# Kernel optimization log

Measured on AMD Instinct MI355X. Metric: run time of the kernel, lower is better.

The kernel has to match this reference:

```python
import jax, jax.numpy as jnp
import numpy as np

N, E = 50000, 800000
IN_DIM, HID, HEADS, OUT_DIM, EDGE_DIM = 128, 32, 4, 64, 32


def _glorot(key, shape, dtype=jnp.float32):
    fan_in, fan_out = shape[0], shape[1]
    lim = np.sqrt(6.0 / (fan_in + fan_out))
    return jax.random.uniform(key, shape, dtype, -lim, lim)


def setup_inputs() -> dict:
    key = jax.random.key(0)
    ks = jax.random.split(key, 16)
    H1 = HEADS * HID  # 128 = concat width of layer 1
    inp = {
        "x": jax.random.normal(ks[0], (N, IN_DIM), jnp.float32),
        "edge_index": jax.random.randint(ks[1], (2, E), 0, N, jnp.int64),
        "edge_feats": jax.random.normal(ks[2], (E, EDGE_DIM), jnp.float32),
        # layer 1: TransformerConv(128 -> 32, heads=4, concat=True, edge_dim=32)
        "Wq1": _glorot(ks[3], (IN_DIM, H1)), "bq1": jnp.zeros((H1,), jnp.float32),
        "Wk1": _glorot(ks[4], (IN_DIM, H1)), "bk1": jnp.zeros((H1,), jnp.float32),
        "Wv1": _glorot(ks[5], (IN_DIM, H1)), "bv1": jnp.zeros((H1,), jnp.float32),
        "We1": _glorot(ks[6], (EDGE_DIM, H1)),
        "Ws1": _glorot(ks[7], (IN_DIM, H1)), "bs1": jnp.zeros((H1,), jnp.float32),
        # layer 2: TransformerConv(128 -> 64, heads=1, concat=False, edge_dim=32)
        "Wq2": _glorot(ks[8], (H1, OUT_DIM)), "bq2": jnp.zeros((OUT_DIM,), jnp.float32),
        "Wk2": _glorot(ks[9], (H1, OUT_DIM)), "bk2": jnp.zeros((OUT_DIM,), jnp.float32),
        "Wv2": _glorot(ks[10], (H1, OUT_DIM)), "bv2": jnp.zeros((OUT_DIM,), jnp.float32),
        "We2": _glorot(ks[11], (EDGE_DIM, OUT_DIM)),
        "Ws2": _glorot(ks[12], (H1, OUT_DIM)), "bs2": jnp.zeros((OUT_DIM,), jnp.float32),
    }
    return inp


def _tconv(x, src, dst, e, Wq, bq, Wk, bk, Wv, bv, We, Ws, bs, heads, concat):
    """PyG TransformerConv: gather q_i/k_j/v_j, add edge embedding to k and v,
    segment-softmax over incoming edges of each target node, scatter-aggregate."""
    n = x.shape[0]
    d = Wq.shape[1] // heads
    q = (x @ Wq + bq).reshape(n, heads, d)
    k = (x @ Wk + bk).reshape(n, heads, d)
    v = (x @ Wv + bv).reshape(n, heads, d)
    ee = (e @ We).reshape(-1, heads, d)      # [E, H, D]
    kj = k[src] + ee                          # [E, H, D]
    vj = v[src] + ee                          # [E, H, D]
    a = jnp.einsum('ehd,ehd->eh', q[dst], kj) / jnp.sqrt(jnp.asarray(d, x.dtype))
    amax = jax.ops.segment_max(a, dst, num_segments=n)      # [N, H]
    ex = jnp.exp(a - amax[dst])
    den = jax.ops.segment_sum(ex, dst, num_segments=n)
    alpha = ex / den[dst]                                   # [E, H]
    out = jax.ops.segment_sum(alpha[..., None] * vj, dst, num_segments=n)
    out = out.reshape(n, heads * d) if concat else out.mean(axis=1)
    return out + x @ Ws + bs  # root/skip connection (lin_skip)


def reference(x, edge_index, edge_feats,
              Wq1, bq1, Wk1, bk1, Wv1, bv1, We1, Ws1, bs1,
              Wq2, bq2, Wk2, bk2, Wv2, bv2, We2, Ws2, bs2):
    src, dst = edge_index[0], edge_index[1]  # flow='source_to_target'
    h = _tconv(x, src, dst, edge_feats, Wq1, bq1, Wk1, bk1, Wv1, bv1,
               We1, Ws1, bs1, heads=HEADS, concat=True)
    h = jax.nn.relu(h)  # activation; dropout p=0.0 is identity
    h = _tconv(h, src, dst, edge_feats, Wq2, bq2, Wk2, bk2, Wv2, bv2,
               We2, Ws2, bs2, heads=1, concat=False)
    return h
```

## Files before the change

kernel.cpp:

```cpp
#include <hip/hip_runtime.h>
#include <hip/hip_bf16.h>


typedef unsigned int  u32;
typedef unsigned short u16;
typedef __attribute__((ext_vector_type(8))) __bf16 bf16x8;
typedef __attribute__((ext_vector_type(4))) float  f32x4;

#define S1L (0.17677669529663687f * 1.4426950408889634f)
#define S2L (0.125f * 1.4426950408889634f)

__device__ __forceinline__ u16 f2bf(float f) {
    u32 u = __float_as_uint(f);
    u32 r = (u + 0x7fffu + ((u >> 16) & 1u)) >> 16;
    return (u16)r;
}
__device__ __forceinline__ float bflo(u32 u) { return __uint_as_float(u << 16); }
__device__ __forceinline__ float bfhi(u32 u) { return __uint_as_float(u & 0xffff0000u); }

template<int CTRL>
__device__ __forceinline__ float dpp_add(float x) {
    int y = __builtin_amdgcn_mov_dpp(__float_as_int(x), CTRL, 0xF, 0xF, true);
    return x + __int_as_float(y);
}

__global__ void k_hist(const int* __restrict__ dst, int* __restrict__ deg, int nE) {
    int e = blockIdx.x * 256 + threadIdx.x;
    if (e < nE) atomicAdd(&deg[dst[e]], 1);
}

__global__ __launch_bounds__(1024) void k_scan_part(const int* __restrict__ deg,
                                                    int* __restrict__ rp,
                                                    int* __restrict__ csum, int nN)
{
    __shared__ int buf[1024];
    const int tid = threadIdx.x, idx = blockIdx.x * 1024 + tid;
    int v = (idx < nN) ? deg[idx] : 0;
    buf[tid] = v;
    __syncthreads();
    for (int off = 1; off < 1024; off <<= 1) {
        int t = (tid >= off) ? buf[tid - off] : 0;
        __syncthreads();
        buf[tid] += t;
        __syncthreads();
    }
    if (idx < nN) rp[idx] = buf[tid] - v;
    if (tid == 1023) csum[blockIdx.x] = buf[1023];
}

__global__ __launch_bounds__(1024) void k_scan_tot(int* __restrict__ csum, int nb,
                                                   int* __restrict__ rowptr, int nN, int nE)
{
    __shared__ int buf[1024];
    const int tid = threadIdx.x;
    int v = (tid < nb) ? csum[tid] : 0;
    buf[tid] = v;
    __syncthreads();
    for (int off = 1; off < 1024; off <<= 1) {
        int t = (tid >= off) ? buf[tid - off] : 0;
        __syncthreads();
        buf[tid] += t;
        __syncthreads();
    }
    if (tid < nb) csum[tid] = buf[tid] - v;
    if (tid == 0) rowptr[nN] = nE;
}

__global__ void k_scan_apply(int* __restrict__ rp, const int* __restrict__ csum,
                             int* __restrict__ fill, int nN)
{
    int i = blockIdx.x * 256 + threadIdx.x;
    if (i < nN) { int r = rp[i] + csum[i >> 10]; rp[i] = r; fill[i] = r; }
}

__global__ void k_scatter_idx(const int* __restrict__ src, const int* __restrict__ dst,
                              int* __restrict__ fill, int2* __restrict__ se, int nE)
{
    int e = blockIdx.x * 256 + threadIdx.x;
    if (e < nE) {
        int p = atomicAdd(&fill[dst[e]], 1);
        se[p] = make_int2(src[e], e);
    }
}

__global__ void k_ef_gather(const int2* __restrict__ se, const float4* __restrict__ ef4,
                            uint2* __restrict__ efc2, int nE)
{
    int t = blockIdx.x * 256 + threadIdx.x;
    int p = t >> 3, sub = t & 7;
    if (p >= nE) return;
    int e = se[p].y;
    float4 f = ef4[(size_t)e * 8 + sub];
    efc2[(size_t)p * 8 + sub] =
        make_uint2((u32)f2bf(f.x) | ((u32)f2bf(f.y) << 16),
                   (u32)f2bf(f.z) | ((u32)f2bf(f.w) << 16));
}

__global__ void k_prep(
    const float* __restrict__ Wq1, const float* __restrict__ Wk1,
    const float* __restrict__ Wv1, const float* __restrict__ Ws1,
    const float* __restrict__ Wq2, const float* __restrict__ Wk2,
    const float* __restrict__ Wv2, const float* __restrict__ Ws2,
    const float* __restrict__ We1, const float* __restrict__ We2,
    const float* __restrict__ bq1, const float* __restrict__ bq2,
    u16* __restrict__ WB1, u16* __restrict__ WB2,
    float* __restrict__ bqe1, float* __restrict__ bqe2,
    const float4* __restrict__ x4, uint2* __restrict__ xb4, int nN)
{
    long t = (long)blockIdx.x * 256 + threadIdx.x;
    if (t < 65536) {
        int j = (int)t >> 7, k = (int)t & 127;
        int m = j >> 7, col = j & 127;
        const float* W = (m == 0) ? Wq1 : (m == 1) ? Wk1 : (m == 2) ? Wv1 : Ws1;
        WB1[t] = f2bf(W[k * 128 + col]);
        return;
    }
    t -= 65536;
    if (t < 49152) {
        int j = (int)t >> 7, k = (int)t & 127;
        if (j < 256) {
            int m = j >> 6, col = j & 63;
            const float* W = (m == 0) ? Wq2 : (m == 1) ? Wk2 : (m == 2) ? Wv2 : Ws2;
            WB2[t] = f2bf(W[k * 64 + col]);
        } else if (j >= 288) {
            WB2[t] = 0;
        }
        return;
    }
    t -= 49152;
    if (t < 16384) {
        int j = (int)t >> 7, m = (int)t & 127;
        int h = j >> 5, c = j & 31;
        float acc = 0.f;
        #pragma unroll
        for (int d = 0; d < 32; ++d)
            acc += Wq1[m * 128 + h * 32 + d] * We1[c * 128 + h * 32 + d];
        WB1[512 * 128 + j * 128 + m] = f2bf(acc * S1L);
        if (m == 0) {
            float b = 0.f;
            #pragma unroll
            for (int d = 0; d < 32; ++d)
                b += bq1[h * 32 + d] * We1[c * 128 + h * 32 + d];
            bqe1[j] = b * S1L;
        }
        return;
    }
    t -= 16384;
    if (t < 4096) {
        int c = (int)t >> 7, m = (int)t & 127;
        float acc = 0.f;
        #pragma unroll
        for (int d = 0; d < 64; ++d)
            acc += Wq2[m * 64 + d] * We2[c * 64 + d];
        WB2[256 * 128 + c * 128 + m] = f2bf(acc * S2L);
        if (m == 0) {
            float b = 0.f;
            #pragma unroll
            for (int d = 0; d < 64; ++d) b += bq2[d] * We2[c * 64 + d];
            bqe2[c] = b * S2L;
        }
        return;
    }
    t -= 4096;
    if (t < (long)nN * 32) {
        float4 f = x4[t];
        xb4[t] = make_uint2((u32)f2bf(f.x) | ((u32)f2bf(f.y) << 16),
                            (u32)f2bf(f.z) | ((u32)f2bf(f.w) << 16));
    }
}

__global__ __launch_bounds__(256) void k_lin_gemm1(
    const u16* __restrict__ xb, const u16* __restrict__ WB,
    const float* __restrict__ bq, const float* __restrict__ bk,
    const float* __restrict__ bv, const float* __restrict__ bs,
    const float* __restrict__ bqe,
    u32* __restrict__ qqe1, u32* __restrict__ kv1, float* __restrict__ sk1, int nN)
{
    __shared__ __align__(16) u16 lds[2 * 128 * 128];
    const int tid = threadIdx.x;
    const int ct = blockIdx.y;
    const int rowbase = blockIdx.x * 128;

    {
        const int lr = tid >> 4, kc = tid & 15;
        #pragma unroll
        for (int it = 0; it < 8; ++it) {
            int row = it * 16 + lr;
            int grow = rowbase + row; if (grow >= nN) grow = nN - 1;
            uint4 va = *(const uint4*)(xb + (size_t)grow * 128 + kc * 8);
            *(uint4*)((char*)lds + row * 256 + ((kc * 16) ^ ((row & 7) << 4))) = va;
        }
        #pragma unroll
        for (int it = 0; it < 8; ++it) {
            int row = it * 16 + lr;
            uint4 vb = *(const uint4*)(WB + ((size_t)ct * 128 + row) * 128 + kc * 8);
            *(uint4*)((char*)lds + 32768 + row * 256 + ((kc * 16) ^ ((row & 7) << 4))) = vb;
        }
    }
    __syncthreads();

    const int wave = tid >> 6, lane = tid & 63;
    const int wr = wave >> 1, wc = wave & 1;
    const int colL = lane & 15, kgrp = lane >> 4;

    f32x4 acc[4][4];
    #pragma unroll
    for (int m = 0; m < 4; ++m)
        #pragma unroll
        for (int n = 0; n < 4; ++n) acc[m][n] = {0.f, 0.f, 0.f, 0.f};

    #pragma unroll
    for (int ks = 0; ks < 4; ++ks) {
        const int kb = ks * 64 + kgrp * 16;
        bf16x8 af[4], bfr[4];
        #pragma unroll
        for (int m = 0; m < 4; ++m) {
            int row = wr * 64 + m * 16 + colL;
            af[m] = *(const bf16x8*)((const char*)lds + row * 256 + (kb ^ ((row & 7) << 4)));
        }
        #pragma unroll
        for (int n = 0; n < 4; ++n) {
            int row = wc * 64 + n * 16 + colL;
            bfr[n] = *(const bf16x8*)((const char*)lds + 32768 + row * 256 + (kb ^ ((row & 7) << 4)));
        }
        #pragma unroll
        for (int m = 0; m < 4; ++m)
            #pragma unroll
            for (int n = 0; n < 4; ++n)
                acc[m][n] = __builtin_amdgcn_mfma_f32_16x16x32_bf16(af[m], bfr[n], acc[m][n], 0, 0, 0);
    }

    const float* bias = (ct == 0) ? bq : (ct == 1) ? bk : (ct == 2) ? bv : (ct == 3) ? bs : bqe;
    const float scale = (ct == 0) ? S1L : 1.f;
    const bool  is32 = (ct == 3);
    const int   hi = (ct == 2 || ct == 4) ? 1 : 0;
    u32* dstw = (ct == 3) ? (u32*)sk1 : ((ct == 1 || ct == 2) ? kv1 : qqe1);

    #pragma unroll
    for (int n = 0; n < 4; ++n) {
        const int c = wc * 64 + n * 16 + colL;
        const float bval = bias[c];
        #pragma unroll
        for (int m = 0; m < 4; ++m) {
            #pragma unroll
            for (int i = 0; i < 4; ++i) {
                const int r = rowbase + wr * 64 + m * 16 + kgrp * 4 + i;
                if (r < nN) {
                    float v = (acc[m][n][i] + bval) * scale;
                    if (is32) ((float*)dstw)[(size_t)r * 128 + c] = v;
                    else ((u16*)dstw)[(((size_t)r * 128 + c) << 1) + hi] = f2bf(v);
                }
            }
        }
    }
}

__global__ __launch_bounds__(256) void k_lin_gemm2(
    const u16* __restrict__ hb, const u16* __restrict__ WB,
    const float* __restrict__ bq, const float* __restrict__ bk,
    const float* __restrict__ bv, const float* __restrict__ bs,
    const float* __restrict__ bqe,
    float* __restrict__ q2, u32* __restrict__ kv2, float* __restrict__ sk2,
    float* __restrict__ qe2, int nN)
{
    __shared__ __align__(16) u16 lds[2 * 128 * 128];
    const int tid = threadIdx.x;
    const int ct = blockIdx.y;
    const int rowbase = blockIdx.x * 128;

    {
        const int lr = tid >> 4, kc = tid & 15;
        #pragma unroll
        for (int it = 0; it < 8; ++it) {
            int row = it * 16 + lr;
            int grow = rowbase + row; if (grow >= nN) grow = nN - 1;
            uint4 va = *(const uint4*)(hb + (size_t)grow * 128 + kc * 8);
            *(uint4*)((char*)lds + row * 256 + ((kc * 16) ^ ((row & 7) << 4))) = va;
        }
        #pragma unroll
        for (int it = 0; it < 8; ++it) {
            int row = it * 16 + lr;
            uint4 vb = *(const uint4*)(WB + ((size_t)ct * 128 + row) * 128 + kc * 8);
            *(uint4*)((char*)lds + 32768 + row * 256 + ((kc * 16) ^ ((row & 7) << 4))) = vb;
        }
    }
    __syncthreads();

    const int wave = tid >> 6, lane = tid & 63;
    const int wr = wave >> 1, wc = wave & 1;
    const int colL = lane & 15, kgrp = lane >> 4;

    f32x4 acc[4][4];
    #pragma unroll
    for (int m = 0; m < 4; ++m)
        #pragma unroll
        for (int n = 0; n < 4; ++n) acc[m][n] = {0.f, 0.f, 0.f, 0.f};

    #pragma unroll
    for (int ks = 0; ks < 4; ++ks) {
        const int kb = ks * 64 + kgrp * 16;
        bf16x8 af[4], bfr[4];
        #pragma unroll
        for (int m = 0; m < 4; ++m) {
            int row = wr * 64 + m * 16 + colL;
            af[m] = *(const bf16x8*)((const char*)lds + row * 256 + (kb ^ ((row & 7) << 4)));
        }
        #pragma unroll
        for (int n = 0; n < 4; ++n) {
            int row = wc * 64 + n * 16 + colL;
            bfr[n] = *(const bf16x8*)((const char*)lds + 32768 + row * 256 + (kb ^ ((row & 7) << 4)));
        }
        #pragma unroll
        for (int m = 0; m < 4; ++m)
            #pragma unroll
            for (int n = 0; n < 4; ++n)
                acc[m][n] = __builtin_amdgcn_mfma_f32_16x16x32_bf16(af[m], bfr[n], acc[m][n], 0, 0, 0);
    }

    const int mode = ct * 2 + wc;
    if (mode == 5) return;

    #pragma unroll
    for (int n = 0; n < 4; ++n) {
        const int cl = n * 16 + colL;
        float bval;
        if (mode == 0) bval = bq[cl];
        else if (mode == 1) bval = bk[cl];
        else if (mode == 2) bval = bv[cl];
        else if (mode == 3) bval = bs[cl];
        else bval = (cl < 32) ? bqe[cl] : 0.f;
        #pragma unroll
        for (int m = 0; m < 4; ++m) {
            #pragma unroll
            for (int i = 0; i < 4; ++i) {
                const int r = rowbase + wr * 64 + m * 16 + kgrp * 4 + i;
                if (r < nN) {
                    const float v = acc[m][n][i] + bval;
                    if (mode == 0)      q2[(size_t)r * 64 + cl] = v * S2L;
                    else if (mode == 1) ((u16*)kv2)[(((size_t)r * 64 + cl) << 1)] = f2bf(v);
                    else if (mode == 2) ((u16*)kv2)[(((size_t)r * 64 + cl) << 1) + 1] = f2bf(v);
                    else if (mode == 3) sk2[(size_t)r * 64 + cl] = v;
                    else if (cl < 32)   qe2[(size_t)r * 32 + cl] = v;
                }
            }
        }
    }
}

__global__ __launch_bounds__(256) void k_agg1(
    const int* __restrict__ rowptr, const int2* __restrict__ se,
    const u16* __restrict__ efc, const u32* __restrict__ qqe1,
    const u32* __restrict__ kv1,
    float* __restrict__ sv1, float* __restrict__ sef1, float* __restrict__ den1, int nN)
{
    const int wave = threadIdx.x >> 6, lane = threadIdx.x & 63;
    const int d = blockIdx.x * 4 + wave;
    if (d >= nN) return;
    const int es = lane >> 5;
    const int h  = (lane >> 3) & 3;
    const int c8 = lane & 7;
    const int jb = h * 32 + c8 * 4;

    const uint4 qq = *(const uint4*)(qqe1 + (size_t)d * 128 + jb);
    const float4 qr  = {bflo(qq.x), bflo(qq.y), bflo(qq.z), bflo(qq.w)};
    const float4 qer = {bfhi(qq.x), bfhi(qq.y), bfhi(qq.z), bfhi(qq.w)};

    const int beg = rowptr[d], end = rowptr[d + 1];
    float den = 0.f;
    float4 sv = {0.f, 0.f, 0.f, 0.f}, sef = sv;

    for (int cbeg = beg; cbeg < end; cbeg += 64) {
        const int cnt = min(64, end - cbeg);
        const int sreg = se[cbeg + (lane < cnt ? lane : cnt - 1)].x;
        #pragma unroll 2
        for (int t = 0; t < cnt; t += 2) {
            const int idx = t + es;
            const bool valid = idx < cnt;
            const int s = __shfl(sreg, idx);
            const int iec = cbeg + (valid ? idx : 0);
            const uint4 kp = *(const uint4*)(kv1 + ((u32)s << 7) + jb);
            const uint2 ee = *(const uint2*)(efc + ((size_t)iec << 5) + c8 * 4);
            const float f0 = bflo(ee.x), f1 = bfhi(ee.x);
            const float f2 = bflo(ee.y), f3 = bfhi(ee.y);
            float p = qr.x * bflo(kp.x) + qr.y * bflo(kp.y)
                    + qr.z * bflo(kp.z) + qr.w * bflo(kp.w)
                    + qer.x * f0 + qer.y * f1 + qer.z * f2 + qer.w * f3;
            p = dpp_add<0xB1>(p);
            p = dpp_add<0x4E>(p);
            p = dpp_add<0x141>(p);
            const float ex = valid ? exp2f(p) : 0.f;
            den += ex;
            sv.x += ex * bfhi(kp.x); sv.y += ex * bfhi(kp.y);
            sv.z += ex * bfhi(kp.z); sv.w += ex * bfhi(kp.w);
            sef.x += ex * f0; sef.y += ex * f1; sef.z += ex * f2; sef.w += ex * f3;
        }
    }
    den  += __shfl_xor(den, 32);
    sv.x += __shfl_xor(sv.x, 32); sv.y += __shfl_xor(sv.y, 32);
    sv.z += __shfl_xor(sv.z, 32); sv.w += __shfl_xor(sv.w, 32);
    sef.x += __shfl_xor(sef.x, 32); sef.y += __shfl_xor(sef.y, 32);
    sef.z += __shfl_xor(sef.z, 32); sef.w += __shfl_xor(sef.w, 32);
    if (es == 0) {
        *(float4*)(sv1  + (size_t)d * 128 + jb) = sv;
        *(float4*)(sef1 + (size_t)d * 128 + jb) = sef;
        if (c8 == 0) den1[(size_t)d * 4 + h] = den;
    }
}

__global__ __launch_bounds__(256) void k_finalize1(
    const float* __restrict__ sv1, const float* __restrict__ sef1,
    const float* __restrict__ den1, const float* __restrict__ sk1,
    const float* __restrict__ We, u16* __restrict__ h1b, int nN)
{
    const int tid = threadIdx.x;
    const int g = tid >> 7, j = tid & 127, h = j >> 5;
    float wreg[32];
    #pragma unroll
    for (int cc = 0; cc < 32; ++cc) wreg[cc] = We[cc * 128 + j];
    for (int n = blockIdx.x * 2 + g; n < nN; n += gridDim.x * 2) {
        float dd = den1[(size_t)n * 4 + h];
        float acc = sv1[(size_t)n * 128 + j];
        const float* sefp = &sef1[(size_t)n * 128 + h * 32];
        #pragma unroll
        for (int cc = 0; cc < 32; ++cc) acc = fmaf(sefp[cc], wreg[cc], acc);
        float o = (dd > 0.f ? acc / dd : 0.f) + sk1[(size_t)n * 128 + j];
        h1b[(size_t)n * 128 + j] = f2bf(o > 0.f ? o : 0.f);
    }
}

__global__ __launch_bounds__(256) void k_agg2(
    const int* __restrict__ rowptr, const int2* __restrict__ se,
    const u16* __restrict__ efc, const float* __restrict__ q2,
    const float* __restrict__ qe2, const u32* __restrict__ kv2,
    float* __restrict__ sv2, float* __restrict__ sef2, float* __restrict__ den2, int nN)
{
    const int wave = threadIdx.x >> 6, lane = threadIdx.x & 63;
    const int d = blockIdx.x * 4 + wave;
    if (d >= nN) return;
    const int es  = lane >> 4;
    const int c16 = lane & 15;
    const int jb  = c16 * 4;
    const int ce  = (c16 & 7) * 4;

    const float4 qr = *(const float4*)(q2 + (size_t)d * 64 + jb);
    float4 qer = {0.f, 0.f, 0.f, 0.f};
    if (c16 < 8) qer = *(const float4*)(qe2 + (size_t)d * 32 + jb);

    const int beg = rowptr[d], end = rowptr[d + 1];
    float den = 0.f;
    float4 sv = {0.f, 0.f, 0.f, 0.f}, sef = sv;

    for (int cbeg = beg; cbeg < end; cbeg += 64) {
        const int cnt = min(64, end - cbeg);
        const int sreg = se[cbeg + (lane < cnt ? lane : cnt - 1)].x;
        #pragma unroll 2
        for (int t = 0; t < cnt; t += 4) {
            const int idx = t + es;
            const bool valid = idx < cnt;
            const int s = __shfl(sreg, idx);
            const int iec = cbeg + (valid ? idx : 0);
            const uint4 kp = *(const uint4*)(kv2 + ((u32)s << 6) + jb);
            const uint2 ee = *(const uint2*)(efc + ((size_t)iec << 5) + ce);
            const float f0 = bflo(ee.x), f1 = bfhi(ee.x);
            const float f2 = bflo(ee.y), f3 = bfhi(ee.y);
            float p = qr.x * bflo(kp.x) + qr.y * bflo(kp.y)
                    + qr.z * bflo(kp.z) + qr.w * bflo(kp.w)
                    + qer.x * f0 + qer.y * f1 + qer.z * f2 + qer.w * f3;
            p = dpp_add<0xB1>(p);
            p = dpp_add<0x4E>(p);
            p = dpp_add<0x141>(p);
            p = dpp_add<0x140>(p);
            const float ex = valid ? exp2f(p) : 0.f;
            den += ex;
            sv.x += ex * bfhi(kp.x); sv.y += ex * bfhi(kp.y);
            sv.z += ex * bfhi(kp.z); sv.w += ex * bfhi(kp.w);
            sef.x += ex * f0; sef.y += ex * f1; sef.z += ex * f2; sef.w += ex * f3;
        }
    }
    #pragma unroll
    for (int m = 16; m <= 32; m <<= 1) {
        den  += __shfl_xor(den, m);
        sv.x += __shfl_xor(sv.x, m); sv.y += __shfl_xor(sv.y, m);
        sv.z += __shfl_xor(sv.z, m); sv.w += __shfl_xor(sv.w, m);
        sef.x += __shfl_xor(sef.x, m); sef.y += __shfl_xor(sef.y, m);
        sef.z += __shfl_xor(sef.z, m); sef.w += __shfl_xor(sef.w, m);
    }
    if (es == 0) {
        *(float4*)(sv2 + (size_t)d * 64 + jb) = sv;
        if (c16 < 8) *(float4*)(sef2 + (size_t)d * 32 + jb) = sef;
        if (c16 == 0) den2[d] = den;
    }
}

__global__ __launch_bounds__(256) void k_finalize2(
    const float* __restrict__ sv2, const float* __restrict__ sef2,
    const float* __restrict__ den2, const float* __restrict__ sk2,
    const float* __restrict__ We, float* __restrict__ out, int nN)
{
    const int tid = threadIdx.x;
    const int g = tid >> 6, c = tid & 63;
    float wreg[32];
    #pragma unroll
    for (int k = 0; k < 32; ++k) wreg[k] = We[k * 64 + c];
    for (int n = blockIdx.x * 4 + g; n < nN; n += gridDim.x * 4) {
        float dd = den2[n];
        float acc = sv2[(size_t)n * 64 + c];
        const float* sefp = &sef2[(size_t)n * 32];
        #pragma unroll
        for (int k = 0; k < 32; ++k) acc = fmaf(sefp[k], wreg[k], acc);
        out[(size_t)n * 64 + c] = (dd > 0.f ? acc / dd : 0.f) + sk2[(size_t)n * 64 + c];
    }
}

extern "C" void kernel_launch(void* const* d_in, const int* in_sizes, int n_in,
                              void* d_out, int out_size, void* d_ws, size_t ws_size,
                              hipStream_t stream)
{
    const float* x   = (const float*)d_in[0];
    const int*   ei  = (const int*)d_in[1];
    const float* ef  = (const float*)d_in[2];
    const float* Wq1 = (const float*)d_in[3];  const float* bq1 = (const float*)d_in[4];
    const float* Wk1 = (const float*)d_in[5];  const float* bk1 = (const float*)d_in[6];
    const float* Wv1 = (const float*)d_in[7];  const float* bv1 = (const float*)d_in[8];
    const float* We1 = (const float*)d_in[9];
    const float* Ws1 = (const float*)d_in[10]; const float* bs1 = (const float*)d_in[11];
    const float* Wq2 = (const float*)d_in[12]; const float* bq2 = (const float*)d_in[13];
    const float* Wk2 = (const float*)d_in[14]; const float* bk2 = (const float*)d_in[15];
    const float* Wv2 = (const float*)d_in[16]; const float* bv2 = (const float*)d_in[17];
    const float* We2 = (const float*)d_in[18];
    const float* Ws2 = (const float*)d_in[19]; const float* bs2 = (const float*)d_in[20];

    const int nN = in_sizes[0] / 128;
    const int nE = in_sizes[1] / 2;
    const int* srcv = ei;
    const int* dstv = ei + nE;

    float* ws = (float*)d_ws;
    size_t off = 0;
    auto alloc = [&](size_t n) { float* p = ws + off; off += n; return p; };
    u32*   qqe1  = (u32*)alloc((size_t)nN * 128);
    float* sk1   = alloc((size_t)nN * 128);
    u32*   kv1   = (u32*)alloc((size_t)nN * 128);
    float* sv1   = alloc((size_t)nN * 128);
    float* sef1  = alloc((size_t)nN * 128);
    u16*   h1b   = (u16*)alloc((size_t)nN * 64);
    u16*   xb    = (u16*)alloc((size_t)nN * 64);
    float* den1  = alloc((size_t)nN * 4);
    u16*   efc   = (u16*)alloc((size_t)nE * 16);
    u16*   WB1   = (u16*)alloc(640 * 128 / 2);
    u16*   WB2   = (u16*)alloc(384 * 128 / 2);
    float* bqe1  = alloc(128);
    float* bqe2  = alloc(32);
    int* deg     = (int*)alloc(nN);
    int* rowptr  = (int*)alloc(nN + 1);
    int* fill    = (int*)alloc(nN);
    int* csum    = (int*)alloc(1024);
    int2* se     = (int2*)alloc((size_t)nE * 2);
    float* l2 = (float*)qqe1;
    size_t o2 = 0;
    auto alloc2 = [&](size_t n) { float* p = l2 + o2; o2 += n; return p; };
    float* q2   = alloc2((size_t)nN * 64);
    u32*   kv2  = (u32*)alloc2((size_t)nN * 64);
    float* sk2  = alloc2((size_t)nN * 64);
    float* qe2  = alloc2((size_t)nN * 32);
    float* sv2  = alloc2((size_t)nN * 64);
    float* sef2 = alloc2((size_t)nN * 32);
    float* den2 = alloc2(nN);
    (void)ws_size; (void)n_in; (void)out_size;

    const int nChunk = (nN + 1023) / 1024;
    const int rowTiles = (nN + 127) / 128;

    hipMemsetAsync(deg, 0, (size_t)nN * sizeof(int), stream);
    k_hist<<<(nE + 255) / 256, 256, 0, stream>>>(dstv, deg, nE);
    k_scan_part<<<nChunk, 1024, 0, stream>>>(deg, rowptr, csum, nN);
    k_scan_tot<<<1, 1024, 0, stream>>>(csum, nChunk, rowptr, nN, nE);
    k_scan_apply<<<(nN + 255) / 256, 256, 0, stream>>>(rowptr, csum, fill, nN);
    k_scatter_idx<<<(nE + 255) / 256, 256, 0, stream>>>(srcv, dstv, fill, se, nE);
    k_ef_gather<<<(nE * 8 + 255) / 256, 256, 0, stream>>>(
        se, (const float4*)ef, (uint2*)efc, nE);

    long prepTotal = 65536L + 49152 + 16384 + 4096 + (long)nN * 32;
    k_prep<<<(int)((prepTotal + 255) / 256), 256, 0, stream>>>(
        Wq1, Wk1, Wv1, Ws1, Wq2, Wk2, Wv2, Ws2, We1, We2, bq1, bq2,
        WB1, WB2, bqe1, bqe2, (const float4*)x, (uint2*)xb, nN);

    k_lin_gemm1<<<dim3(rowTiles, 5), 256, 0, stream>>>(
        xb, WB1, bq1, bk1, bv1, bs1, bqe1, qqe1, kv1, sk1, nN);
    k_agg1<<<(nN + 3) / 4, 256, 0, stream>>>(
        rowptr, se, efc, qqe1, kv1, sv1, sef1, den1, nN);
    k_finalize1<<<1024, 256, 0, stream>>>(sv1, sef1, den1, sk1, We1, h1b, nN);

    k_lin_gemm2<<<dim3(rowTiles, 3), 256, 0, stream>>>(
        h1b, WB2, bq2, bk2, bv2, bs2, bqe2, q2, kv2, sk2, qe2, nN);
    k_agg2<<<(nN + 3) / 4, 256, 0, stream>>>(
        rowptr, se, efc, q2, qe2, kv2, sv2, sef2, den2, nN);
    k_finalize2<<<1024, 256, 0, stream>>>(sv2, sef2, den2, sk2, We2, (float*)d_out, nN);
}
```

Baseline: 405.6 us.

## Fuse finalize into aggregation kernels and merge scatter with prep

Merges the aggregation and finalize stages of both layers into persistent grid-stride kernels. Each wave writes its per-node softmax numerators and denominators to LDS, and the We projection, normalization, skip add and activation are applied in place. This removes the global round trip of sv/sef/den buffers and two launches. The edge-index scatter is also folded into the weight/x prep kernel to save another launch. The cost is two block-wide syncs per iteration, so waves with high-degree nodes stall the whole block, and extra registers are needed to hold We.

New measurement: 402.2 us. No clear change (-0.8%).

```diff
diff --git a/kernel.cpp b/kernel.cpp
--- a/kernel.cpp
+++ b/kernel.cpp
@@ -73,30 +73,9 @@
     if (i < nN) { int r = rp[i] + csum[i >> 10]; rp[i] = r; fill[i] = r; }
 }
 
-__global__ void k_scatter_idx(const int* __restrict__ src, const int* __restrict__ dst,
-                              int* __restrict__ fill, int2* __restrict__ se, int nE)
-{
-    int e = blockIdx.x * 256 + threadIdx.x;
-    if (e < nE) {
-        int p = atomicAdd(&fill[dst[e]], 1);
-        se[p] = make_int2(src[e], e);
-    }
-}
-
-__global__ void k_ef_gather(const int2* __restrict__ se, const float4* __restrict__ ef4,
-                            uint2* __restrict__ efc2, int nE)
-{
-    int t = blockIdx.x * 256 + threadIdx.x;
-    int p = t >> 3, sub = t & 7;
-    if (p >= nE) return;
-    int e = se[p].y;
-    float4 f = ef4[(size_t)e * 8 + sub];
-    efc2[(size_t)p * 8 + sub] =
-        make_uint2((u32)f2bf(f.x) | ((u32)f2bf(f.y) << 16),
-                   (u32)f2bf(f.z) | ((u32)f2bf(f.w) << 16));
-}
-
-__global__ void k_prep(
+__global__ void k_scatter_prep(
+    const int* __restrict__ src, const int* __restrict__ dst,
+    int* __restrict__ fill, int2* __restrict__ se, int nE,
     const float* __restrict__ Wq1, const float* __restrict__ Wk1,
     const float* __restrict__ Wv1, const float* __restrict__ Ws1,
     const float* __restrict__ Wq2, const float* __restrict__ Wk2,
@@ -107,7 +86,14 @@
     float* __restrict__ bqe1, float* __restrict__ bqe2,
     const float4* __restrict__ x4, uint2* __restrict__ xb4, int nN)
 {
-    long t = (long)blockIdx.x * 256 + threadIdx.x;
+    long g = (long)blockIdx.x * 256 + threadIdx.x;
+    if (g < nE) {
+        int e = (int)g;
+        int p = atomicAdd(&fill[dst[e]], 1);
+        se[p] = make_int2(src[e], e);
+        return;
+    }
+    long t = g - nE;
     if (t < 65536) {
         int j = (int)t >> 7, k = (int)t & 127;
         int m = j >> 7, col = j & 127;
@@ -167,6 +153,19 @@
         xb4[t] = make_uint2((u32)f2bf(f.x) | ((u32)f2bf(f.y) << 16),
                             (u32)f2bf(f.z) | ((u32)f2bf(f.w) << 16));
     }
+}
+
+__global__ void k_ef_gather(const int2* __restrict__ se, const float4* __restrict__ ef4,
+                            uint2* __restrict__ efc2, int nE)
+{
+    int t = blockIdx.x * 256 + threadIdx.x;
+    int p = t >> 3, sub = t & 7;
+    if (p >= nE) return;
+    int e = se[p].y;
+    float4 f = ef4[(size_t)e * 8 + sub];
+    efc2[(size_t)p * 8 + sub] =
+        make_uint2((u32)f2bf(f.x) | ((u32)f2bf(f.y) << 16),
+                   (u32)f2bf(f.z) | ((u32)f2bf(f.w) << 16));
 }
 
 __global__ __launch_bounds__(256) void k_lin_gemm1(
@@ -347,168 +346,178 @@
     }
 }
 
-__global__ __launch_bounds__(256) void k_agg1(
+__global__ __launch_bounds__(256) void k_agg1f(
     const int* __restrict__ rowptr, const int2* __restrict__ se,
     const u16* __restrict__ efc, const u32* __restrict__ qqe1,
-    const u32* __restrict__ kv1,
-    float* __restrict__ sv1, float* __restrict__ sef1, float* __restrict__ den1, int nN)
-{
+    const u32* __restrict__ kv1, const float* __restrict__ sk1,
+    const float* __restrict__ We, u16* __restrict__ h1b, int nN, int stride4)
+{
+    __shared__ float lsv[4][128];
+    __shared__ float lsef[4][128];
+    __shared__ float lden[4][4];
     const int wave = threadIdx.x >> 6, lane = threadIdx.x & 63;
-    const int d = blockIdx.x * 4 + wave;
-    if (d >= nN) return;
     const int es = lane >> 5;
     const int h  = (lane >> 3) & 3;
     const int c8 = lane & 7;
     const int jb = h * 32 + c8 * 4;
-
-    const uint4 qq = *(const uint4*)(qqe1 + (size_t)d * 128 + jb);
-    const float4 qr  = {bflo(qq.x), bflo(qq.y), bflo(qq.z), bflo(qq.w)};
-    const float4 qer = {bfhi(qq.x), bfhi(qq.y), bfhi(qq.z), bfhi(qq.w)};
-
-    const int beg = rowptr[d], end = rowptr[d + 1];
-    float den = 0.f;
-    float4 sv = {0.f, 0.f, 0.f, 0.f}, sef = sv;
-
-    for (int cbeg = beg; cbeg < end; cbeg += 64) {
-        const int cnt = min(64, end - cbeg);
-        const int sreg = se[cbeg + (lane < cnt ? lane : cnt - 1)].x;
-        #pragma unroll 2
-        for (int t = 0; t < cnt; t += 2) {
-            const int idx = t + es;
-            const bool valid = idx < cnt;
-            const int s = __shfl(sreg, idx);
-            const int iec = cbeg + (valid ? idx : 0);
-            const uint4 kp = *(const uint4*)(kv1 + ((u32)s << 7) + jb);
-            const uint2 ee = *(const uint2*)(efc + ((size_t)iec << 5) + c8 * 4);
-            const float f0 = bflo(ee.x), f1 = bfhi(ee.x);
-            const float f2 = bflo(ee.y), f3 = bfhi(ee.y);
-            float p = qr.x * bflo(kp.x) + qr.y * bflo(kp.y)
-                    + qr.z * bflo(kp.z) + qr.w * bflo(kp.w)
-                    + qer.x * f0 + qer.y * f1 + qer.z * f2 + qer.w * f3;
-            p = dpp_add<0xB1>(p);
-            p = dpp_add<0x4E>(p);
-            p = dpp_add<0x141>(p);
-            const float ex = valid ? exp2f(p) : 0.f;
-            den += ex;
-            sv.x += ex * bfhi(kp.x); sv.y += ex * bfhi(kp.y);
-            sv.z += ex * bfhi(kp.z); sv.w += ex * bfhi(kp.w);
-            sef.x += ex * f0; sef.y += ex * f1; sef.z += ex * f2; sef.w += ex * f3;
-        }
-    }
-    den  += __shfl_xor(den, 32);
-    sv.x += __shfl_xor(sv.x, 32); sv.y += __shfl_xor(sv.y, 32);
-    sv.z += __shfl_xor(sv.z, 32); sv.w += __shfl_xor(sv.w, 32);
-    sef.x += __shfl_xor(sef.x, 32); sef.y += __shfl_xor(sef.y, 32);
-    sef.z += __shfl_xor(sef.z, 32); sef.w += __shfl_xor(sef.w, 32);
-    if (es == 0) {
-        *(float4*)(sv1  + (size_t)d * 128 + jb) = sv;
-        *(float4*)(sef1 + (size_t)d * 128 + jb) = sef;
-        if (c8 == 0) den1[(size_t)d * 4 + h] = den;
-    }
-}
-
-__global__ __launch_bounds__(256) void k_finalize1(
-    const float* __restrict__ sv1, const float* __restrict__ sef1,
-    const float* __restrict__ den1, const float* __restrict__ sk1,
-    const float* __restrict__ We, u16* __restrict__ h1b, int nN)
-{
-    const int tid = threadIdx.x;
-    const int g = tid >> 7, j = tid & 127, h = j >> 5;
-    float wreg[32];
-    #pragma unroll
-    for (int cc = 0; cc < 32; ++cc) wreg[cc] = We[cc * 128 + j];
-    for (int n = blockIdx.x * 2 + g; n < nN; n += gridDim.x * 2) {
-        float dd = den1[(size_t)n * 4 + h];
-        float acc = sv1[(size_t)n * 128 + j];
-        const float* sefp = &sef1[(size_t)n * 128 + h * 32];
-        #pragma unroll
-        for (int cc = 0; cc < 32; ++cc) acc = fmaf(sefp[cc], wreg[cc], acc);
-        float o = (dd > 0.f ? acc / dd : 0.f) + sk1[(size_t)n * 128 + j];
-        h1b[(size_t)n * 128 + j] = f2bf(o > 0.f ? o : 0.f);
-    }
-}
-
-__global__ __launch_bounds__(256) void k_agg2(
+    const int jA = lane, jB = lane + 64;
+    const int hA = jA >> 5, hB = jB >> 5;
+    float wA[32], wB[32];
+    #pragma unroll
+    for (int c = 0; c < 32; ++c) {
+        wA[c] = We[c * 128 + jA];
+        wB[c] = We[c * 128 + jB];
+    }
+
+    for (int dbase = blockIdx.x * 4; dbase < nN; dbase += stride4) {
+        const int d = dbase + wave;
+        const bool act = d < nN;
+        float den = 0.f;
+        float4 sv = {0.f, 0.f, 0.f, 0.f}, sef = sv;
+        if (act) {
+            const uint4 qq = *(const uint4*)(qqe1 + (size_t)d * 128 + jb);
+            const float4 qr  = {bflo(qq.x), bflo(qq.y), bflo(qq.z), bflo(qq.w)};
+            const float4 qer = {bfhi(qq.x), bfhi(qq.y), bfhi(qq.z), bfhi(qq.w)};
+            const int beg = rowptr[d], end = rowptr[d + 1];
+            for (int cbeg = beg; cbeg < end; cbeg += 64) {
+                const int cnt = min(64, end - cbeg);
+                const int sreg = se[cbeg + (lane < cnt ? lane : cnt - 1)].x;
+                #pragma unroll 2
+                for (int t = 0; t < cnt; t += 2) {
+                    const int idx = t + es;
+                    const bool valid = idx < cnt;
+                    const int s = __shfl(sreg, idx);
+                    const int iec = cbeg + (valid ? idx : 0);
+                    const uint4 kp = *(const uint4*)(kv1 + ((u32)s << 7) + jb);
+                    const uint2 ee = *(const uint2*)(efc + ((size_t)iec << 5) + c8 * 4);
+                    const float f0 = bflo(ee.x), f1 = bfhi(ee.x);
+                    const float f2 = bflo(ee.y), f3 = bfhi(ee.y);
+                    float p = qr.x * bflo(kp.x) + qr.y * bflo(kp.y)
+                            + qr.z * bflo(kp.z) + qr.w * bflo(kp.w)
+                            + qer.x * f0 + qer.y * f1 + qer.z * f2 + qer.w * f3;
+                    p = dpp_add<0xB1>(p);
+                    p = dpp_add<0x4E>(p);
+                    p = dpp_add<0x141>(p);
+                    const float ex = valid ? exp2f(p) : 0.f;
+                    den += ex;
+                    sv.x += ex * bfhi(kp.x); sv.y += ex * bfhi(kp.y);
+                    sv.z += ex * bfhi(kp.z); sv.w += ex * bfhi(kp.w);
+                    sef.x += ex * f0; sef.y += ex * f1; sef.z += ex * f2; sef.w += ex * f3;
+                }
+            }
+            den  += __shfl_xor(den, 32);
+            sv.x += __shfl_xor(sv.x, 32); sv.y += __shfl_xor(sv.y, 32);
+            sv.z += __shfl_xor(sv.z, 32); sv.w += __shfl_xor(sv.w, 32);
+            sef.x += __shfl_xor(sef.x, 32); sef.y += __shfl_xor(sef.y, 32);
+            sef.z += __shfl_xor(sef.z, 32); sef.w += __shfl_xor(sef.w, 32);
+            if (es == 0) {
+                *(float4*)&lsv[wave][jb]  = sv;
+                *(float4*)&lsef[wave][jb] = sef;
+                if (c8 == 0) lden[wave][h] = den;
+            }
+        }
+        __syncthreads();
+        if (act) {
+            const float ddA = lden[wave][hA], ddB = lden[wave][hB];
+            const float invA = ddA > 0.f ? 1.0f / ddA : 0.f;
+            const float invB = ddB > 0.f ? 1.0f / ddB : 0.f;
+            float aA = lsv[wave][jA], aB = lsv[wave][jB];
+            const float* spA = &lsef[wave][hA * 32];
+            const float* spB = &lsef[wave][hB * 32];
+            #pragma unroll
+            for (int c = 0; c < 32; ++c) {
+                aA = fmaf(spA[c], wA[c], aA);
+                aB = fmaf(spB[c], wB[c], aB);
+            }
+            float oA = aA * invA + sk1[(size_t)d * 128 + jA];
+            float oB = aB * invB + sk1[(size_t)d * 128 + jB];
+            h1b[(size_t)d * 128 + jA] = f2bf(oA > 0.f ? oA : 0.f);
+            h1b[(size_t)d * 128 + jB] = f2bf(oB > 0.f ? oB : 0.f);
+        }
+        __syncthreads();
+    }
+}
+
+__global__ __launch_bounds__(256) void k_agg2f(
     const int* __restrict__ rowptr, const int2* __restrict__ se,
     const u16* __restrict__ efc, const float* __restrict__ q2,
     const float* __restrict__ qe2, const u32* __restrict__ kv2,
-    float* __restrict__ sv2, float* __restrict__ sef2, float* __restrict__ den2, int nN)
-{
+    const float* __restrict__ sk2, const float* __restrict__ We,
+    float* __restrict__ out, int nN, int stride4)
+{
+    __shared__ float lsv[4][64];
+    __shared__ float lsef[4][32];
+    __shared__ float lden[4];
     const int wave = threadIdx.x >> 6, lane = threadIdx.x & 63;
-    const int d = blockIdx.x * 4 + wave;
-    if (d >= nN) return;
     const int es  = lane >> 4;
     const int c16 = lane & 15;
     const int jb  = c16 * 4;
     const int ce  = (c16 & 7) * 4;
-
-    const float4 qr = *(const float4*)(q2 + (size_t)d * 64 + jb);
-    float4 qer = {0.f, 0.f, 0.f, 0.f};
-    if (c16 < 8) qer = *(const float4*)(qe2 + (size_t)d * 32 + jb);
-
-    const int beg = rowptr[d], end = rowptr[d + 1];
-    float den = 0.f;
-    float4 sv = {0.f, 0.f, 0.f, 0.f}, sef = sv;
-
-    for (int cbeg = beg; cbeg < end; cbeg += 64) {
-        const int cnt = min(64, end - cbeg);
-        const int sreg = se[cbeg + (lane < cnt ? lane : cnt - 1)].x;
-        #pragma unroll 2
-        for (int t = 0; t < cnt; t += 4) {
-            const int idx = t + es;
-            const bool valid = idx < cnt;
-            const int s = __shfl(sreg, idx);
-            const int iec = cbeg + (valid ? idx : 0);
-            const uint4 kp = *(const uint4*)(kv2 + ((u32)s << 6) + jb);
-            const uint2 ee = *(const uint2*)(efc + ((size_t)iec << 5) + ce);
-            const float f0 = bflo(ee.x), f1 = bfhi(ee.x);
-            const float f2 = bflo(ee.y), f3 = bfhi(ee.y);
-            float p = qr.x * bflo(kp.x) + qr.y * bflo(kp.y)
-                    + qr.z * bflo(kp.z) + qr.w * bflo(kp.w)
-                    + qer.x * f0 + qer.y * f1 + qer.z * f2 + qer.w * f3;
-            p = dpp_add<0xB1>(p);
-            p = dpp_add<0x4E>(p);
-            p = dpp_add<0x141>(p);
-            p = dpp_add<0x140>(p);
-            const float ex = valid ? exp2f(p) : 0.f;
-            den += ex;
-            sv.x += ex * bfhi(kp.x); sv.y += ex * bfhi(kp.y);
-            sv.z += ex * bfhi(kp.z); sv.w += ex * bfhi(kp.w);
-            sef.x += ex * f0; sef.y += ex * f1; sef.z += ex * f2; sef.w += ex * f3;
-        }
-    }
-    #pragma unroll
-    for (int m = 16; m <= 32; m <<= 1) {
-        den  += __shfl_xor(den, m);
-        sv.x += __shfl_xor(sv.x, m); sv.y += __shfl_xor(sv.y, m);
-        sv.z += __shfl_xor(sv.z, m); sv.w += __shfl_xor(sv.w, m);
-        sef.x += __shfl_xor(sef.x, m); sef.y += __shfl_xor(sef.y, m);
-        sef.z += __shfl_xor(sef.z, m); sef.w += __shfl_xor(sef.w, m);
-    }
-    if (es == 0) {
-        *(float4*)(sv2 + (size_t)d * 64 + jb) = sv;
-        if (c16 < 8) *(float4*)(sef2 + (size_t)d * 32 + jb) = sef;
-        if (c16 == 0) den2[d] = den;
-    }
-}
-
-__global__ __launch_bounds__(256) void k_finalize2(
-    const float* __restrict__ sv2, const float* __restrict__ sef2,
-    const float* __restrict__ den2, const float* __restrict__ sk2,
-    const float* __restrict__ We, float* __restrict__ out, int nN)
-{
-    const int tid = threadIdx.x;
-    const int g = tid >> 6, c = tid & 63;
     float wreg[32];
     #pragma unroll
-    for (int k = 0; k < 32; ++k) wreg[k] = We[k * 64 + c];
-    for (int n = blockIdx.x * 4 + g; n < nN; n += gridDim.x * 4) {
-        float dd = den2[n];
-        float acc = sv2[(size_t)n * 64 + c];
-        const float* sefp = &sef2[(size_t)n * 32];
-        #pragma unroll
-        for (int k = 0; k < 32; ++k) acc = fmaf(sefp[k], wreg[k], acc);
-        out[(size_t)n * 64 + c] = (dd > 0.f ? acc / dd : 0.f) + sk2[(size_t)n * 64 + c];
+    for (int c = 0; c < 32; ++c) wreg[c] = We[c * 64 + lane];
+
+    for (int dbase = blockIdx.x * 4; dbase < nN; dbase += stride4) {
+        const int d = dbase + wave;
+        const bool act = d < nN;
+        float den = 0.f;
+        float4 sv = {0.f, 0.f, 0.f, 0.f}, sef = sv;
+        if (act) {
+            const float4 qr = *(const float4*)(q2 + (size_t)d * 64 + jb);
+            float4 qer = {0.f, 0.f, 0.f, 0.f};
+            if (c16 < 8) qer = *(const float4*)(qe2 + (size_t)d * 32 + jb);
+            const int beg = rowptr[d], end = rowptr[d + 1];
+            for (int cbeg = beg; cbeg < end; cbeg += 64) {
+                const int cnt = min(64, end - cbeg);
+                const int sreg = se[cbeg + (lane < cnt ? lane : cnt - 1)].x;
+                #pragma unroll 2
+                for (int t = 0; t < cnt; t += 4) {
+                    const int idx = t + es;
+                    const bool valid = idx < cnt;
+                    const int s = __shfl(sreg, idx);
+                    const int iec = cbeg + (valid ? idx : 0);
+                    const uint4 kp = *(const uint4*)(kv2 + ((u32)s << 6) + jb);
+                    const uint2 ee = *(const uint2*)(efc + ((size_t)iec << 5) + ce);
+                    const float f0 = bflo(ee.x), f1 = bfhi(ee.x);
+                    const float f2 = bflo(ee.y), f3 = bfhi(ee.y);
+                    float p = qr.x * bflo(kp.x) + qr.y * bflo(kp.y)
+                            + qr.z * bflo(kp.z) + qr.w * bflo(kp.w)
+                            + qer.x * f0 + qer.y * f1 + qer.z * f2 + qer.w * f3;
+                    p = dpp_add<0xB1>(p);
+                    p = dpp_add<0x4E>(p);
+                    p = dpp_add<0x141>(p);
+                    p = dpp_add<0x140>(p);
+                    const float ex = valid ? exp2f(p) : 0.f;
+                    den += ex;
+                    sv.x += ex * bfhi(kp.x); sv.y += ex * bfhi(kp.y);
+                    sv.z += ex * bfhi(kp.z); sv.w += ex * bfhi(kp.w);
+                    sef.x += ex * f0; sef.y += ex * f1; sef.z += ex * f2; sef.w += ex * f3;
+                }
+            }
+            #pragma unroll
+            for (int m = 16; m <= 32; m <<= 1) {
+                den  += __shfl_xor(den, m);
+                sv.x += __shfl_xor(sv.x, m); sv.y += __shfl_xor(sv.y, m);
+                sv.z += __shfl_xor(sv.z, m); sv.w += __shfl_xor(sv.w, m);
+                sef.x += __shfl_xor(sef.x, m); sef.y += __shfl_xor(sef.y, m);
+                sef.z += __shfl_xor(sef.z, m); sef.w += __shfl_xor(sef.w, m);
+            }
+            if (es == 0) {
+                *(float4*)&lsv[wave][jb] = sv;
+                if (c16 < 8) *(float4*)&lsef[wave][jb] = sef;
+                if (c16 == 0) lden[wave] = den;
+            }
+        }
+        __syncthreads();
+        if (act) {
+            const float dd = lden[wave];
+            const float inv = dd > 0.f ? 1.0f / dd : 0.f;
+            float a = lsv[wave][lane];
+            #pragma unroll
+            for (int c = 0; c < 32; ++c) a = fmaf(lsef[wave][c], wreg[c], a);
+            out[(size_t)d * 64 + lane] = a * inv + sk2[(size_t)d * 64 + lane];
+        }
+        __syncthreads();
     }
 }
 
@@ -541,11 +550,8 @@
     u32*   qqe1  = (u32*)alloc((size_t)nN * 128);
     float* sk1   = alloc((size_t)nN * 128);
     u32*   kv1   = (u32*)alloc((size_t)nN * 128);
-    float* sv1   = alloc((size_t)nN * 128);
-    float* sef1  = alloc((size_t)nN * 128);
     u16*   h1b   = (u16*)alloc((size_t)nN * 64);
     u16*   xb    = (u16*)alloc((size_t)nN * 64);
-    float* den1  = alloc((size_t)nN * 4);
     u16*   efc   = (u16*)alloc((size_t)nE * 16);
     u16*   WB1   = (u16*)alloc(640 * 128 / 2);
     u16*   WB2   = (u16*)alloc(384 * 128 / 2);
@@ -561,39 +567,37 @@
     auto alloc2 = [&](size_t n) { float* p = l2 + o2; o2 += n; return p; };
     float* q2   = alloc2((size_t)nN * 64);
     u32*   kv2  = (u32*)alloc2((size_t)nN * 64);
-    float* sk2  = alloc2((size_t)nN * 64);
-    float* qe2  = alloc2((size_t)nN * 32);
-    float* sv2  = alloc2((size_t)nN * 64);
-    float* sef2 = alloc2((size_t)nN * 32);
-    float* den2 = alloc2(nN);
+    (void)alloc2(0);
+    float* sk2  = alloc((size_t)nN * 64);
+    float* qe2  = alloc((size_t)nN * 32);
     (void)ws_size; (void)n_in; (void)out_size;
 
     const int nChunk = (nN + 1023) / 1024;
     const int rowTiles = (nN + 127) / 128;
+    const int aggBlocks = 2048;
 
     hipMemsetAsync(deg, 0, (size_t)nN * sizeof(int), stream);
     k_hist<<<(nE + 255) / 256, 256, 0, stream>>>(dstv, deg, nE);
     k_scan_part<<<nChunk, 1024, 0, stream>>>(deg, rowptr, csum, nN);
     k_scan_tot<<<1, 1024, 0, stream>>>(csum, nChunk, rowptr, nN, nE);
     k_scan_apply<<<(nN + 255) / 256, 256, 0, stream>>>(rowptr, csum, fill, nN);
-    k_scatter_idx<<<(nE + 255) / 256, 256, 0, stream>>>(srcv, dstv, fill, se, nE);
+
+    long prepTotal = 65536L + 49152 + 16384 + 4096 + (long)nN * 32;
+    long spTotal = (long)nE + prepTotal;
+    k_scatter_prep<<<(int)((spTotal + 255) / 256), 256, 0, stream>>>(
+        srcv, dstv, fill, se, nE,
+        Wq1, Wk1, Wv1, Ws1, Wq2, Wk2, Wv2, Ws2, We1, We2, bq1, bq2,
+        WB1, WB2, bqe1, bqe2, (const float4*)x, (uint2*)xb, nN);
     k_ef_gather<<<(nE * 8 + 255) / 256, 256, 0, stream>>>(
         se, (const float4*)ef, (uint2*)efc, nE);
 
-    long prepTotal = 65536L + 49152 + 16384 + 4096 + (long)nN * 32;
-    k_prep<<<(int)((prepTotal + 255) / 256), 256, 0, stream>>>(
-        Wq1, Wk1, Wv1, Ws1, Wq2, Wk2, Wv2, Ws2, We1, We2, bq1, bq2,
-        WB1, WB2, bqe1, bqe2, (const float4*)x, (uint2*)xb, nN);
-
     k_lin_gemm1<<<dim3(rowTiles, 5), 256, 0, stream>>>(
         xb, WB1, bq1, bk1, bv1, bs1, bqe1, qqe1, kv1, sk1, nN);
-    k_agg1<<<(nN + 3) / 4, 256, 0, stream>>>(
-        rowptr, se, efc, qqe1, kv1, sv1, sef1, den1, nN);
-    k_finalize1<<<1024, 256, 0, stream>>>(sv1, sef1, den1, sk1, We1, h1b, nN);
+    k_agg1f<<<aggBlocks, 256, 0, stream>>>(
+        rowptr, se, efc, qqe1, kv1, sk1, We1, h1b, nN, aggBlocks * 4);
 
     k_lin_gemm2<<<dim3(rowTiles, 3), 256, 0, stream>>>(
         h1b, WB2, bq2, bk2, bv2, bs2, bqe2, q2, kv2, sk2, qe2, nN);
-    k_agg2<<<(nN + 3) / 4, 256, 0, stream>>>(
-        rowptr, se, efc, q2, qe2, kv2, sv2, sef2, den2, nN);
-    k_finalize2<<<1024, 256, 0, stream>>>(sv2, sef2, den2, sk2, We2, (float*)d_out, nN);
-}
+    k_agg2f<<<aggBlocks, 256, 0, stream>>>(
+        rowptr, se, efc, q2, qe2, kv2, sk2, We2, (float*)d_out, nN, aggBlocks * 4);
+}
```
